# Kernel tuning notes

Measured on AMD Instinct MI355X. Metric: run time of the kernel, lower is better.

Reference implementation:

```python
import jax, jax.numpy as jnp
import numpy as np

B, S, D = 512, 200, 512
NQ, NC, NQD, NCD = 10000, 500, 101, 101


def _linear_params(key, fin, fout):
    # torch nn.Linear default init: U(-1/sqrt(fin), 1/sqrt(fin)); store W as (in,out)
    k1, k2 = jax.random.split(key)
    bound = 1.0 / np.sqrt(fin)
    W = jax.random.uniform(k1, (fin, fout), minval=-bound, maxval=bound, dtype=jnp.float32)
    b = jax.random.uniform(k2, (fout,), minval=-bound, maxval=bound, dtype=jnp.float32)
    return W, b


def setup_inputs() -> dict:
    key = jax.random.key(0)
    ks = jax.random.split(key, 16)
    inp = {
        'question_seq': jax.random.randint(ks[0], (B, S), 0, NQ),
        'concept_seq': jax.random.randint(ks[1], (B, S), 0, NC),
        'question_diff_seq': jax.random.randint(ks[2], (B, S), 0, NQD),
        'concept_diff_seq': jax.random.randint(ks[3], (B, S), 0, NCD),
        'correct_seq': jax.random.randint(ks[4], (B, S), 0, 2),
        'E_q': jax.random.normal(ks[5], (NQ, D), dtype=jnp.float32),
        'E_c': jax.random.normal(ks[6], (NC, D), dtype=jnp.float32),
        'E_qd': jax.random.normal(ks[7], (NQD, D), dtype=jnp.float32),
        'E_cd': jax.random.normal(ks[8], (NCD, D), dtype=jnp.float32),
        'E_corr': jax.random.normal(ks[9], (2, D), dtype=jnp.float32),
    }
    inp['W_x'], inp['b_x'] = _linear_params(ks[10], 4 * D, D)
    inp['W_s1'], inp['b_s1'] = _linear_params(ks[11], D, D)
    inp['W_s2'], inp['b_s2'] = _linear_params(ks[12], D, D)
    inp['W_p1'], inp['b_p1'] = _linear_params(ks[13], 2 * D, D)
    inp['W_p2'], inp['b_p2'] = _linear_params(ks[14], 2 * D, D)
    inp['W_ki'], inp['b_ki'] = _linear_params(ks[15], 4 * D, D)
    # h_pre: xavier_uniform on a (B, D) tensor -> U(-a, a), a = sqrt(6/(B+D))
    a = np.sqrt(6.0 / (B + D))
    inp['h0'] = jax.random.uniform(jax.random.key(1), (B, D), minval=-a, maxval=a, dtype=jnp.float32)
    return inp


def reference(question_seq, concept_seq, question_diff_seq, concept_diff_seq, correct_seq,
              E_q, E_c, E_qd, E_cd, E_corr,
              W_x, b_x, W_s1, b_s1, W_s2, b_s2, W_p1, b_p1, W_p2, b_p2, W_ki, b_ki, h0):
    # embedding lookups: [B, S, D]
    qe = E_q[question_seq]
    ce = E_c[concept_seq]
    qde = E_qd[question_diff_seq]
    cde = E_cd[concept_diff_seq]
    corr = E_corr[correct_seq]

    # generate_x_MLP applied to concat of 4 embeddings, vectorized over all t: [B, S, D]
    x_all = jnp.concatenate([qe, ce, qde, cde], axis=-1) @ W_x + b_x

    # time-major slices for scan over t = 0 .. S-2
    def tm(a):  # [B, S, D] -> [S, B, D]
        return jnp.swapaxes(a, 0, 1)

    xs = (tm(x_all)[:-1], tm(x_all)[1:], tm(corr)[:-1], tm(qde)[:-1], tm(cde)[:-1])

    def step(h_pre, t_in):
        x_t, x_next, ce_t, qd_t, cd_t = t_in
        d = x_t - h_pre
        # dropout in eval mode = identity
        sdf = jax.nn.sigmoid(d @ W_s1 + b_s1) * jnp.tanh(d @ W_s2 + b_s2)
        pka_in = jnp.concatenate([sdf, ce_t], axis=-1)
        pka = jax.nn.sigmoid(pka_in @ W_p1 + b_p1) * jnp.tanh(pka_in @ W_p2 + b_p2)
        ki_in = jnp.concatenate([h_pre, ce_t, qd_t, cd_t], axis=-1)
        gamma = jax.nn.sigmoid(ki_in @ W_ki + b_ki)
        h = gamma * h_pre + (1.0 - gamma) * pka
        y_t = jax.nn.sigmoid(jnp.sum(x_next * h, axis=-1))  # [B]
        return h, y_t

    _, y_seq = jax.lax.scan(step, h0, xs)  # y_seq: [S-1, B]
    y = jnp.concatenate([y_seq.T, jnp.zeros((question_seq.shape[0], 1), dtype=y_seq.dtype)], axis=1)
    return y  # [B, S], last column 0 as in the torch code
```

## Files before the change

kernel.cpp:

```cpp
#include <hip/hip_runtime.h>


typedef unsigned short u16;
using f32x4 = __attribute__((ext_vector_type(4))) float;
using bf16x8 = __attribute__((ext_vector_type(8))) short;

#define DEV static __device__ __forceinline__

#define Bv 512
#define Sv 200

DEV u16 f2bf(float f) {
  unsigned int u = __float_as_uint(f);
  unsigned int r = (u + 0x7fffu + ((u >> 16) & 1u)) >> 16;
  return (u16)r;
}
DEV float bf2f(u16 h) { return __uint_as_float(((unsigned int)h) << 16); }
DEV float sigm(float x) { return 1.0f / (1.0f + __expf(-x)); }
DEV float tanh_(float x) {
  x = fmaxf(fminf(x, 15.f), -15.f);
  float e = __expf(2.0f * x);
  return (e - 1.0f) / (e + 1.0f);
}
DEV f32x4 MF(bf16x8 a, bf16x8 b, f32x4 c) {
  return __builtin_amdgcn_mfma_f32_16x16x32_bf16(a, b, c, 0, 0, 0);
}

union LDU { f32x4 f; bf16x8 b; };
DEV void ld16v(f32x4* d, const u16* p) {
  asm volatile("global_load_dwordx4 %0, %1, off sc1" : "=v"(*d) : "v"(p));
}
DEV void st2v(u16* p, u16 v) {
  unsigned w = v;
  asm volatile("global_store_short %0, %1, off sc1" : : "v"(p), "v"(w) : "memory");
}
DEV void waitv0() {
  asm volatile("s_waitcnt vmcnt(0)" ::: "memory");
  __builtin_amdgcn_sched_barrier(0);
}

template <int NB, bool AF32>
DEV void gemm_tiles(const void* __restrict__ Aptr, int mvalid,
                    const u16* __restrict__ BT0, const u16* __restrict__ BT1,
                    u16* ldsA, u16* ldsB0, u16* ldsB1, int tid,
                    f32x4* acc0, f32x4* acc1) {
  const int lane = tid & 63, wid = tid >> 6;
  const int fr = lane & 15, fq = lane >> 4;
  const int srow = tid >> 2, sseg = tid & 3;

  for (int kt = 0; kt < 16; ++kt) {
    const int k0 = kt * 32;
    {
      bf16x8 pack;
      if constexpr (AF32) {
        if (srow < mvalid) {
          const float4* ap = (const float4*)((const float*)Aptr + (size_t)srow * 512 + k0 + sseg * 8);
          float4 v0 = ap[0], v1 = ap[1];
          pack[0] = (short)f2bf(v0.x); pack[1] = (short)f2bf(v0.y);
          pack[2] = (short)f2bf(v0.z); pack[3] = (short)f2bf(v0.w);
          pack[4] = (short)f2bf(v1.x); pack[5] = (short)f2bf(v1.y);
          pack[6] = (short)f2bf(v1.z); pack[7] = (short)f2bf(v1.w);
        } else {
          for (int j = 0; j < 8; ++j) pack[j] = 0;
        }
      } else {
        pack = *(const bf16x8*)((const u16*)Aptr + (size_t)srow * 512 + k0 + sseg * 8);
      }
      *(bf16x8*)&ldsA[srow * 40 + sseg * 8] = pack;
      *(bf16x8*)&ldsB0[srow * 40 + sseg * 8] =
          *(const bf16x8*)(BT0 + (size_t)srow * 512 + k0 + sseg * 8);
      if constexpr (NB == 2)
        *(bf16x8*)&ldsB1[srow * 40 + sseg * 8] =
            *(const bf16x8*)(BT1 + (size_t)srow * 512 + k0 + sseg * 8);
    }
    __syncthreads();
    bf16x8 a = *(const bf16x8*)&ldsA[(wid * 16 + fr) * 40 + fq * 8];
#pragma unroll
    for (int ni = 0; ni < 4; ++ni) {
      bf16x8 b0 = *(const bf16x8*)&ldsB0[(ni * 16 + fr) * 40 + fq * 8];
      acc0[ni] = MF(a, b0, acc0[ni]);
      if constexpr (NB == 2) {
        bf16x8 b1 = *(const bf16x8*)&ldsB1[(ni * 16 + fr) * 40 + fq * 8];
        acc1[ni] = MF(a, b1, acc1[ni]);
      }
    }
    __syncthreads();
  }
}

template <bool F32OUT>
__global__ __launch_bounds__(256) void gemm_table_k(const float* __restrict__ A, int M,
                                                    const u16* __restrict__ BT,
                                                    const float* __restrict__ bias,
                                                    void* __restrict__ C) {
  __shared__ u16 ldsA[64 * 40], ldsB[64 * 40];
  const int m0 = blockIdx.x * 64, n0 = blockIdx.y * 64;
  const int tid = threadIdx.x;
  f32x4 acc[4] = {};
  gemm_tiles<1, true>(A + (size_t)m0 * 512, M - m0, BT + (size_t)n0 * 512, nullptr,
                      ldsA, ldsB, nullptr, tid, acc, nullptr);
  const int lane = tid & 63, wid = tid >> 6, fr = lane & 15, fq = lane >> 4;
#pragma unroll
  for (int ni = 0; ni < 4; ++ni) {
    int col = n0 + ni * 16 + fr;
    float bv = bias ? bias[col] : 0.f;
#pragma unroll
    for (int r = 0; r < 4; ++r) {
      int row = m0 + wid * 16 + fq * 4 + r;
      if (row < M) {
        float v = acc[ni][r] + bv;
        if constexpr (F32OUT)
          ((float*)C)[(size_t)row * 512 + col] = v;
        else
          ((u16*)C)[(size_t)row * 512 + col] = f2bf(v);
      }
    }
  }
}

__global__ __launch_bounds__(256) void convT_k(const float* __restrict__ src, u16* __restrict__ dst) {
  __shared__ float tile[32][33];
  const int bi = blockIdx.x, bj = blockIdx.y;
  const int tx = threadIdx.x & 31, ty = threadIdx.x >> 5;
#pragma unroll
  for (int r = 0; r < 4; ++r)
    tile[ty + 8 * r][tx] = src[(size_t)(bj * 32 + ty + 8 * r) * 512 + bi * 32 + tx];
  __syncthreads();
#pragma unroll
  for (int r = 0; r < 4; ++r)
    dst[(size_t)(bi * 32 + ty + 8 * r) * 512 + bj * 32 + tx] = f2bf(tile[tx][ty + 8 * r]);
}

__global__ __launch_bounds__(256) void seqT_k(
    const int* __restrict__ q, const int* __restrict__ c, const int* __restrict__ qd,
    const int* __restrict__ cd, const int* __restrict__ corr,
    int* __restrict__ qT, int* __restrict__ cT, int* __restrict__ qdT,
    int* __restrict__ cdT, int* __restrict__ corrT) {
  const int i = blockIdx.x * 256 + threadIdx.x;
  const int b = i / Sv, t = i % Sv;
  const int o = t * Bv + b;
  qT[o] = q[i]; cT[o] = c[i]; qdT[o] = qd[i]; cdT[o] = cd[i]; corrT[o] = corr[i];
}

__global__ __launch_bounds__(256) void prologue_k(
    const float* __restrict__ h0, const int* __restrict__ qT, const int* __restrict__ cT,
    const int* __restrict__ qdT, const int* __restrict__ cdT,
    const float* __restrict__ XQ, const float* __restrict__ XC, const float* __restrict__ XQD,
    const float* __restrict__ XCD, u16* __restrict__ hb, u16* __restrict__ d_buf,
    unsigned* __restrict__ flags) {
  const int i = blockIdx.x * 256 + threadIdx.x;
  if (i < 4096) flags[i] = 0u;
  const int b = i >> 9, col = i & 511;
  float h = h0[i];
  int qi = qT[b], cci = cT[b], qdi = qdT[b], cdi = cdT[b];
  float x = XQ[(size_t)qi * 512 + col] + XC[(size_t)cci * 512 + col] +
            XQD[(size_t)qdi * 512 + col] + XCD[(size_t)cdi * 512 + col];
  hb[i] = f2bf(h);
  d_buf[i] = f2bf(x - h);
}

DEV void load_wslice32(const u16* __restrict__ src, u16* dst, int n0, int tid) {
  for (int i = tid; i < 2048; i += 256) {
    int q = i & 3, kc = (i >> 2) & 15, c = i >> 6;
    int slot = c * 4 + (q ^ (c & 3) ^ ((c >> 2) & 3));
    *(bf16x8*)&dst[kc * 1024 + slot * 8] =
        *(const bf16x8*)&src[(size_t)(n0 + c) * 512 + kc * 32 + q * 8];
  }
}

DEV void mg_arrive(unsigned* myslot, unsigned phase, int tid) {
  waitv0();
  __syncthreads();
  __builtin_amdgcn_fence(__ATOMIC_RELEASE, "workgroup");
  if (tid == 0)
    __hip_atomic_store(myslot, phase, __ATOMIC_RELAXED, __HIP_MEMORY_SCOPE_AGENT);
}
DEV void mg_wait(unsigned* mgslots, unsigned phase, int tid) {
  if (tid < 16) {
    while (__hip_atomic_load(&mgslots[tid * 16], __ATOMIC_RELAXED,
                             __HIP_MEMORY_SCOPE_AGENT) < phase)
      __builtin_amdgcn_s_sleep(0);
  }
  __syncthreads();
  __builtin_amdgcn_fence(__ATOMIC_ACQUIRE, "workgroup");
}

__global__ __launch_bounds__(256, 1) void scan_k(
    const u16* __restrict__ Ws1T, const u16* __restrict__ Ws2T, const u16* __restrict__ WkihT,
    const u16* __restrict__ Wp1aT, const u16* __restrict__ Wp2aT,
    const float* __restrict__ b_s1, const float* __restrict__ b_s2,
    const u16* __restrict__ Kcorr, const u16* __restrict__ Kqd, const u16* __restrict__ Kcd,
    const u16* __restrict__ P1c, const u16* __restrict__ P2c,
    const int* __restrict__ qT, const int* __restrict__ cT, const int* __restrict__ qdT,
    const int* __restrict__ cdT, const int* __restrict__ corrT,
    const float* __restrict__ XQ, const float* __restrict__ XC, const float* __restrict__ XQD,
    const float* __restrict__ XCD, const float* __restrict__ h0,
    u16* __restrict__ sdf, u16* __restrict__ dbuf, u16* __restrict__ hb,
    float* __restrict__ dotpart, unsigned* __restrict__ flags) {
  __shared__ u16 wlds[32768];
  const int bid = blockIdx.x;
  const int mg = (bid & 7) | ((bid >> 7) << 3);
  const int ns = (bid >> 3) & 15;
  const int n0 = ns * 32;
  const int tid = threadIdx.x, lane = tid & 63, w = tid >> 6;
  const int rt = w >> 1, ct = w & 1;
  const int fr = lane & 15, fq = lane >> 4;

  load_wslice32(Ws1T, wlds,          n0, tid);
  load_wslice32(Ws2T, wlds + 16384,  n0, tid);

  const int col = n0 + ct * 16 + fr;
  const float bs1 = b_s1[col], bs2 = b_s2[col];
  const float kco0 = bf2f(Kcorr[col]), kco1 = bf2f(Kcorr[512 + col]);
  const float p1c0 = bf2f(P1c[col]),   p1c1 = bf2f(P1c[512 + col]);
  const float p2c0 = bf2f(P2c[col]),   p2c1 = bf2f(P2c[512 + col]);

  const int crow0 = mg * 32 + rt * 16 + fq * 4;
  const size_t aoff = (size_t)(mg * 32 + rt * 16 + fr) * 512 + fq * 8;
  const int slotr = (ct * 16 + fr) * 4 + (fq ^ (fr & 3) ^ ((fr >> 2) & 3));
  const u16* wb = wlds + slotr * 8;

  bf16x8 wkf[16], wp1f[16], wp2f[16];
#pragma unroll
  for (int kc = 0; kc < 16; ++kc) {
    wkf[kc]  = *(const bf16x8*)(WkihT + (size_t)col * 512 + kc * 32 + fq * 8);
    wp1f[kc] = *(const bf16x8*)(Wp1aT + (size_t)col * 512 + kc * 32 + fq * 8);
    wp2f[kc] = *(const bf16x8*)(Wp2aT + (size_t)col * 512 + kc * 32 + fq * 8);
  }

  unsigned* myslot  = flags + (mg * 16 + ns) * 16;
  unsigned* mgslots = flags + mg * 16 * 16;

  float hl[4];
#pragma unroll
  for (int r = 0; r < 4; ++r) hl[r] = h0[(size_t)(crow0 + r) * 512 + col];
  int cis[4];
  float kbias[4];
#pragma unroll
  for (int r = 0; r < 4; ++r) {
    const int row = crow0 + r;
    int ci = corrT[row], qdi = qdT[row], cdi = cdT[row];
    cis[r] = ci;
    kbias[r] = (ci ? kco1 : kco0) + bf2f(Kqd[qdi * 512 + col]) + bf2f(Kcd[cdi * 512 + col]);
  }
  __syncthreads();

  for (int t = 0; t < Sv - 1; ++t) {
    LDU av[16], ah[16];
    __builtin_amdgcn_sched_barrier(0);
#pragma unroll
    for (int kc = 0; kc < 16; ++kc) ld16v(&av[kc].f, dbuf + aoff + kc * 32);
#pragma unroll
    for (int kc = 0; kc < 16; ++kc) ld16v(&ah[kc].f, hb + aoff + kc * 32);
    waitv0();
    f32x4 a1 = {}, a2 = {}, ag = {};
#pragma unroll
    for (int kc = 0; kc < 16; ++kc) {
      a1 = MF(av[kc].b, *(const bf16x8*)(wb + kc * 1024), a1);
      a2 = MF(av[kc].b, *(const bf16x8*)(wb + 16384 + kc * 1024), a2);
      ag = MF(ah[kc].b, wkf[kc], ag);
    }
    float g[4];
#pragma unroll
    for (int r = 0; r < 4; ++r) {
      g[r] = sigm(ag[r] + kbias[r]);
      st2v(&sdf[(size_t)(crow0 + r) * 512 + col], f2bf(sigm(a1[r] + bs1) * tanh_(a2[r] + bs2)));
    }
    mg_arrive(myslot, (unsigned)(2 * t + 1), tid);
    float xv[4];
#pragma unroll
    for (int r = 0; r < 4; ++r) {
      const int row = crow0 + r;
      int qi   = qT[(t + 1) * Bv + row];
      int cci  = cT[(t + 1) * Bv + row];
      int qdi2 = qdT[(t + 1) * Bv + row];
      int cdi2 = cdT[(t + 1) * Bv + row];
      xv[r] = XQ[(size_t)qi * 512 + col] + XC[(size_t)cci * 512 + col] +
              XQD[(size_t)qdi2 * 512 + col] + XCD[(size_t)cdi2 * 512 + col];
    }
    mg_wait(mgslots, (unsigned)(2 * t + 1), tid);

    LDU as[16];
    __builtin_amdgcn_sched_barrier(0);
#pragma unroll
    for (int kc = 0; kc < 16; ++kc) ld16v(&as[kc].f, sdf + aoff + kc * 32);
    waitv0();
    f32x4 ap1 = {}, ap2 = {};
#pragma unroll
    for (int kc = 0; kc < 16; ++kc) {
      ap1 = MF(as[kc].b, wp1f[kc], ap1);
      ap2 = MF(as[kc].b, wp2f[kc], ap2);
    }
    float dots[4];
#pragma unroll
    for (int r = 0; r < 4; ++r) {
      const int row = crow0 + r;
      float pka = sigm(ap1[r] + (cis[r] ? p1c1 : p1c0)) *
                  tanh_(ap2[r] + (cis[r] ? p2c1 : p2c0));
      float hn = g[r] * hl[r] + (1.f - g[r]) * pka;
      hl[r] = hn;
      st2v(&hb[(size_t)row * 512 + col],   f2bf(hn));
      st2v(&dbuf[(size_t)row * 512 + col], f2bf(xv[r] - hn));
      dots[r] = xv[r] * hn;
    }
    mg_arrive(myslot, (unsigned)(2 * t + 2), tid);
#pragma unroll
    for (int r = 0; r < 4; ++r) {
      float v = dots[r];
      v += __shfl_xor(v, 1);
      v += __shfl_xor(v, 2);
      v += __shfl_xor(v, 4);
      v += __shfl_xor(v, 8);
      if (fr == 0) dotpart[((size_t)t * Bv + crow0 + r) * 32 + ns * 2 + ct] = v;
    }
    if (t < Sv - 2) {
#pragma unroll
      for (int r = 0; r < 4; ++r) {
        const int row = crow0 + r;
        int ci = corrT[(t + 1) * Bv + row];
        int qdi = qdT[(t + 1) * Bv + row];
        int cdi = cdT[(t + 1) * Bv + row];
        cis[r] = ci;
        kbias[r] = (ci ? kco1 : kco0) + bf2f(Kqd[qdi * 512 + col]) +
                   bf2f(Kcd[cdi * 512 + col]);
      }
    }
    mg_wait(mgslots, (unsigned)(2 * t + 2), tid);
  }
}

__global__ __launch_bounds__(256) void finalize_k(const float* __restrict__ dotpart,
                                                  float* __restrict__ y) {
  const int i = blockIdx.x * 256 + threadIdx.x;
  const int b = i / Sv, t = i % Sv;
  float v = 0.f;
  if (t < Sv - 1) {
    const float4* p = (const float4*)&dotpart[((size_t)t * Bv + b) * 32];
    float s = 0.f;
#pragma unroll
    for (int k = 0; k < 8; ++k) {
      float4 q = p[k];
      s += q.x + q.y + q.z + q.w;
    }
    v = sigm(s);
  }
  y[i] = v;
}

extern "C" void kernel_launch(void* const* d_in, const int* in_sizes, int n_in,
                              void* d_out, int out_size, void* d_ws, size_t ws_size,
                              hipStream_t stream) {
  (void)in_sizes; (void)n_in; (void)out_size; (void)ws_size;
  const int* q_seq    = (const int*)d_in[0];
  const int* c_seq    = (const int*)d_in[1];
  const int* qd_seq   = (const int*)d_in[2];
  const int* cd_seq   = (const int*)d_in[3];
  const int* corr_seq = (const int*)d_in[4];
  const float* E_q    = (const float*)d_in[5];
  const float* E_c    = (const float*)d_in[6];
  const float* E_qd   = (const float*)d_in[7];
  const float* E_cd   = (const float*)d_in[8];
  const float* E_corr = (const float*)d_in[9];
  const float* W_x  = (const float*)d_in[10];
  const float* b_x  = (const float*)d_in[11];
  const float* W_s1 = (const float*)d_in[12];
  const float* b_s1 = (const float*)d_in[13];
  const float* W_s2 = (const float*)d_in[14];
  const float* b_s2 = (const float*)d_in[15];
  const float* W_p1 = (const float*)d_in[16];
  const float* b_p1 = (const float*)d_in[17];
  const float* W_p2 = (const float*)d_in[18];
  const float* b_p2 = (const float*)d_in[19];
  const float* W_ki = (const float*)d_in[20];
  const float* b_ki = (const float*)d_in[21];
  const float* h0   = (const float*)d_in[22];
  float* y = (float*)d_out;

  char* ws = (char*)d_ws;
  size_t off = 0;
  auto alloc = [&](size_t bytes) -> void* {
    void* p = ws + off;
    off += (bytes + 255) & ~(size_t)255;
    return p;
  };
  const size_t WSZ = 512 * 512 * sizeof(u16);
  u16* WxTq  = (u16*)alloc(WSZ);
  u16* WxTc  = (u16*)alloc(WSZ);
  u16* WxTqd = (u16*)alloc(WSZ);
  u16* WxTcd = (u16*)alloc(WSZ);
  u16* Ws1T  = (u16*)alloc(WSZ);
  u16* Ws2T  = (u16*)alloc(WSZ);
  u16* WkihT = (u16*)alloc(WSZ);
  u16* WkiTco = (u16*)alloc(WSZ);
  u16* WkiTqd = (u16*)alloc(WSZ);
  u16* WkiTcd = (u16*)alloc(WSZ);
  u16* Wp1aT = (u16*)alloc(WSZ);
  u16* Wp1hT = (u16*)alloc(WSZ);
  u16* Wp2aT = (u16*)alloc(WSZ);
  u16* Wp2hT = (u16*)alloc(WSZ);
  float* XQf  = (float*)alloc((size_t)10000 * 512 * 4);
  float* XCf  = (float*)alloc((size_t)500 * 512 * 4);
  float* XQDf = (float*)alloc((size_t)101 * 512 * 4);
  float* XCDf = (float*)alloc((size_t)101 * 512 * 4);
  u16* Kcorr = (u16*)alloc((size_t)2 * 512 * 2);
  u16* Kqd   = (u16*)alloc((size_t)101 * 512 * 2);
  u16* Kcd   = (u16*)alloc((size_t)101 * 512 * 2);
  u16* P1c   = (u16*)alloc((size_t)2 * 512 * 2);
  u16* P2c   = (u16*)alloc((size_t)2 * 512 * 2);
  u16* sdf   = (u16*)alloc((size_t)512 * 512 * 2);
  u16* d_buf = (u16*)alloc((size_t)512 * 512 * 2);
  u16* hb    = (u16*)alloc((size_t)512 * 512 * 2);
  float* dotpart = (float*)alloc((size_t)199 * 512 * 32 * 4);
  int* qT    = (int*)alloc((size_t)Sv * Bv * 4);
  int* cT    = (int*)alloc((size_t)Sv * Bv * 4);
  int* qdT   = (int*)alloc((size_t)Sv * Bv * 4);
  int* cdT   = (int*)alloc((size_t)Sv * Bv * 4);
  int* corrT = (int*)alloc((size_t)Sv * Bv * 4);
  unsigned* flags = (unsigned*)alloc(8192 * 4);

  dim3 blk(256);
  dim3 tg(16, 16);
  convT_k<<<tg, blk, 0, stream>>>(W_x + 0 * 512 * 512, WxTq);
  convT_k<<<tg, blk, 0, stream>>>(W_x + 1 * 512 * 512, WxTc);
  convT_k<<<tg, blk, 0, stream>>>(W_x + 2 * 512 * 512, WxTqd);
  convT_k<<<tg, blk, 0, stream>>>(W_x + 3 * 512 * 512, WxTcd);
  convT_k<<<tg, blk, 0, stream>>>(W_s1, Ws1T);
  convT_k<<<tg, blk, 0, stream>>>(W_s2, Ws2T);
  convT_k<<<tg, blk, 0, stream>>>(W_ki + 0 * 512 * 512, WkihT);
  convT_k<<<tg, blk, 0, stream>>>(W_ki + 1 * 512 * 512, WkiTco);
  convT_k<<<tg, blk, 0, stream>>>(W_ki + 2 * 512 * 512, WkiTqd);
  convT_k<<<tg, blk, 0, stream>>>(W_ki + 3 * 512 * 512, WkiTcd);
  convT_k<<<tg, blk, 0, stream>>>(W_p1 + 0 * 512 * 512, Wp1aT);
  convT_k<<<tg, blk, 0, stream>>>(W_p1 + 1 * 512 * 512, Wp1hT);
  convT_k<<<tg, blk, 0, stream>>>(W_p2 + 0 * 512 * 512, Wp2aT);
  convT_k<<<tg, blk, 0, stream>>>(W_p2 + 1 * 512 * 512, Wp2hT);

  gemm_table_k<true><<<dim3(157, 8), blk, 0, stream>>>(E_q, 10000, WxTq, nullptr, XQf);
  gemm_table_k<true><<<dim3(8, 8), blk, 0, stream>>>(E_c, 500, WxTc, b_x, XCf);
  gemm_table_k<true><<<dim3(2, 8), blk, 0, stream>>>(E_qd, 101, WxTqd, nullptr, XQDf);
  gemm_table_k<true><<<dim3(2, 8), blk, 0, stream>>>(E_cd, 101, WxTcd, nullptr, XCDf);
  gemm_table_k<false><<<dim3(1, 8), blk, 0, stream>>>(E_corr, 2, WkiTco, b_ki, Kcorr);
  gemm_table_k<false><<<dim3(2, 8), blk, 0, stream>>>(E_qd, 101, WkiTqd, nullptr, Kqd);
  gemm_table_k<false><<<dim3(2, 8), blk, 0, stream>>>(E_cd, 101, WkiTcd, nullptr, Kcd);
  gemm_table_k<false><<<dim3(1, 8), blk, 0, stream>>>(E_corr, 2, Wp1hT, b_p1, P1c);
  gemm_table_k<false><<<dim3(1, 8), blk, 0, stream>>>(E_corr, 2, Wp2hT, b_p2, P2c);

  seqT_k<<<dim3(400), blk, 0, stream>>>(q_seq, c_seq, qd_seq, cd_seq, corr_seq,
                                        qT, cT, qdT, cdT, corrT);
  prologue_k<<<dim3(1024), blk, 0, stream>>>(h0, qT, cT, qdT, cdT, XQf, XCf, XQDf, XCDf,
                                             hb, d_buf, flags);

  {
    const u16 *a0 = Ws1T, *a1 = Ws2T, *a2 = WkihT, *a3 = Wp1aT, *a4 = Wp2aT;
    const float *a5 = b_s1, *a6 = b_s2;
    const u16 *a7 = Kcorr, *a8 = Kqd, *a9 = Kcd, *a10 = P1c, *a11 = P2c;
    const int *a12 = qT, *a13 = cT, *a14 = qdT, *a15 = cdT, *a16 = corrT;
    const float *a17 = XQf, *a18 = XCf, *a19 = XQDf, *a20 = XCDf, *a21 = h0;
    u16 *a22 = sdf, *a23 = d_buf, *a24 = hb;
    float* a25 = dotpart;
    unsigned* a26 = flags;
    void* args[] = {&a0, &a1, &a2, &a3, &a4, &a5, &a6, &a7, &a8, &a9, &a10, &a11,
                    &a12, &a13, &a14, &a15, &a16, &a17, &a18, &a19, &a20, &a21,
                    &a22, &a23, &a24, &a25, &a26};
    hipError_t e = hipLaunchCooperativeKernel((void*)scan_k, dim3(256), dim3(256),
                                              args, 0, stream);
    if (e != hipSuccess) {
      scan_k<<<dim3(256), dim3(256), 0, stream>>>(Ws1T, Ws2T, WkihT, Wp1aT, Wp2aT,
                                                  b_s1, b_s2, Kcorr, Kqd, Kcd, P1c, P2c,
                                                  qT, cT, qdT, cdT, corrT,
                                                  XQf, XCf, XQDf, XCDf, h0,
                                                  sdf, d_buf, hb, dotpart, flags);
    }
  }

  finalize_k<<<dim3(400), blk, 0, stream>>>(dotpart, y);
}
```

Measured before the change: 2.452 ms.

## Split d@W_s into precomputed x-table projections minus h@W_s

Uses linearity so that (x - h)@W_s1 and (x - h)@W_s2 become x@W_s minus h@W_s. The x@W_s part is precomputed per embedding table (q, c, qd, cd, with the bias folded into the c table) and gathered per step. Inside the scan the same h fragments now feed all three MFMA chains, so the per-step d buffer no longer has to be loaded and stored. The cost is eight extra table GEMMs, including two over the 10000-row question table, plus eight extra bf16 gathers per row per step. Summing four bf16-rounded partial products also changes rounding behaviour.

```diff
diff --git a/kernel.cpp b/kernel.cpp
--- a/kernel.cpp
+++ b/kernel.cpp
@@ -143,20 +143,10 @@
 }
 
 __global__ __launch_bounds__(256) void prologue_k(
-    const float* __restrict__ h0, const int* __restrict__ qT, const int* __restrict__ cT,
-    const int* __restrict__ qdT, const int* __restrict__ cdT,
-    const float* __restrict__ XQ, const float* __restrict__ XC, const float* __restrict__ XQD,
-    const float* __restrict__ XCD, u16* __restrict__ hb, u16* __restrict__ d_buf,
-    unsigned* __restrict__ flags) {
+    const float* __restrict__ h0, u16* __restrict__ hb, unsigned* __restrict__ flags) {
   const int i = blockIdx.x * 256 + threadIdx.x;
   if (i < 4096) flags[i] = 0u;
-  const int b = i >> 9, col = i & 511;
-  float h = h0[i];
-  int qi = qT[b], cci = cT[b], qdi = qdT[b], cdi = cdT[b];
-  float x = XQ[(size_t)qi * 512 + col] + XC[(size_t)cci * 512 + col] +
-            XQD[(size_t)qdi * 512 + col] + XCD[(size_t)cdi * 512 + col];
-  hb[i] = f2bf(h);
-  d_buf[i] = f2bf(x - h);
+  hb[i] = f2bf(h0[i]);
 }
 
 DEV void load_wslice32(const u16* __restrict__ src, u16* dst, int n0, int tid) {
@@ -188,14 +178,17 @@
 __global__ __launch_bounds__(256, 1) void scan_k(
     const u16* __restrict__ Ws1T, const u16* __restrict__ Ws2T, const u16* __restrict__ WkihT,
     const u16* __restrict__ Wp1aT, const u16* __restrict__ Wp2aT,
-    const float* __restrict__ b_s1, const float* __restrict__ b_s2,
     const u16* __restrict__ Kcorr, const u16* __restrict__ Kqd, const u16* __restrict__ Kcd,
     const u16* __restrict__ P1c, const u16* __restrict__ P2c,
+    const u16* __restrict__ XQS1, const u16* __restrict__ XQS2,
+    const u16* __restrict__ XCS1, const u16* __restrict__ XCS2,
+    const u16* __restrict__ XQDS1, const u16* __restrict__ XQDS2,
+    const u16* __restrict__ XCDS1, const u16* __restrict__ XCDS2,
     const int* __restrict__ qT, const int* __restrict__ cT, const int* __restrict__ qdT,
     const int* __restrict__ cdT, const int* __restrict__ corrT,
     const float* __restrict__ XQ, const float* __restrict__ XC, const float* __restrict__ XQD,
     const float* __restrict__ XCD, const float* __restrict__ h0,
-    u16* __restrict__ sdf, u16* __restrict__ dbuf, u16* __restrict__ hb,
+    u16* __restrict__ sdf, u16* __restrict__ hb,
     float* __restrict__ dotpart, unsigned* __restrict__ flags) {
   __shared__ u16 wlds[32768];
   const int bid = blockIdx.x;
@@ -210,7 +203,6 @@
   load_wslice32(Ws2T, wlds + 16384,  n0, tid);
 
   const int col = n0 + ct * 16 + fr;
-  const float bs1 = b_s1[col], bs2 = b_s2[col];
   const float kco0 = bf2f(Kcorr[col]), kco1 = bf2f(Kcorr[512 + col]);
   const float p1c0 = bf2f(P1c[col]),   p1c1 = bf2f(P1c[512 + col]);
   const float p2c0 = bf2f(P2c[col]),   p2c1 = bf2f(P2c[512 + col]);
@@ -234,37 +226,43 @@
   float hl[4];
 #pragma unroll
   for (int r = 0; r < 4; ++r) hl[r] = h0[(size_t)(crow0 + r) * 512 + col];
+
+  float xs1[4], xs2[4], kbias[4];
   int cis[4];
-  float kbias[4];
 #pragma unroll
   for (int r = 0; r < 4; ++r) {
     const int row = crow0 + r;
-    int ci = corrT[row], qdi = qdT[row], cdi = cdT[row];
+    int qi = qT[row], cci = cT[row], qdi = qdT[row], cdi = cdT[row];
+    int ci = corrT[row];
+    xs1[r] = bf2f(XQS1[(size_t)qi * 512 + col]) + bf2f(XCS1[(size_t)cci * 512 + col]) +
+             bf2f(XQDS1[(size_t)qdi * 512 + col]) + bf2f(XCDS1[(size_t)cdi * 512 + col]);
+    xs2[r] = bf2f(XQS2[(size_t)qi * 512 + col]) + bf2f(XCS2[(size_t)cci * 512 + col]) +
+             bf2f(XQDS2[(size_t)qdi * 512 + col]) + bf2f(XCDS2[(size_t)cdi * 512 + col]);
     cis[r] = ci;
     kbias[r] = (ci ? kco1 : kco0) + bf2f(Kqd[qdi * 512 + col]) + bf2f(Kcd[cdi * 512 + col]);
   }
   __syncthreads();
 
   for (int t = 0; t < Sv - 1; ++t) {
-    LDU av[16], ah[16];
+    LDU ah[16];
     __builtin_amdgcn_sched_barrier(0);
-#pragma unroll
-    for (int kc = 0; kc < 16; ++kc) ld16v(&av[kc].f, dbuf + aoff + kc * 32);
 #pragma unroll
     for (int kc = 0; kc < 16; ++kc) ld16v(&ah[kc].f, hb + aoff + kc * 32);
     waitv0();
     f32x4 a1 = {}, a2 = {}, ag = {};
 #pragma unroll
     for (int kc = 0; kc < 16; ++kc) {
-      a1 = MF(av[kc].b, *(const bf16x8*)(wb + kc * 1024), a1);
-      a2 = MF(av[kc].b, *(const bf16x8*)(wb + 16384 + kc * 1024), a2);
+      a1 = MF(ah[kc].b, *(const bf16x8*)(wb + kc * 1024), a1);
+      a2 = MF(ah[kc].b, *(const bf16x8*)(wb + 16384 + kc * 1024), a2);
       ag = MF(ah[kc].b, wkf[kc], ag);
     }
     float g[4];
 #pragma unroll
     for (int r = 0; r < 4; ++r) {
       g[r] = sigm(ag[r] + kbias[r]);
-      st2v(&sdf[(size_t)(crow0 + r) * 512 + col], f2bf(sigm(a1[r] + bs1) * tanh_(a2[r] + bs2)));
+      float u1 = xs1[r] - a1[r];
+      float u2 = xs2[r] - a2[r];
+      st2v(&sdf[(size_t)(crow0 + r) * 512 + col], f2bf(sigm(u1) * tanh_(u2)));
     }
     mg_arrive(myslot, (unsigned)(2 * t + 1), tid);
     float xv[4];
@@ -277,6 +275,10 @@
       int cdi2 = cdT[(t + 1) * Bv + row];
       xv[r] = XQ[(size_t)qi * 512 + col] + XC[(size_t)cci * 512 + col] +
               XQD[(size_t)qdi2 * 512 + col] + XCD[(size_t)cdi2 * 512 + col];
+      xs1[r] = bf2f(XQS1[(size_t)qi * 512 + col]) + bf2f(XCS1[(size_t)cci * 512 + col]) +
+               bf2f(XQDS1[(size_t)qdi2 * 512 + col]) + bf2f(XCDS1[(size_t)cdi2 * 512 + col]);
+      xs2[r] = bf2f(XQS2[(size_t)qi * 512 + col]) + bf2f(XCS2[(size_t)cci * 512 + col]) +
+               bf2f(XQDS2[(size_t)qdi2 * 512 + col]) + bf2f(XCDS2[(size_t)cdi2 * 512 + col]);
     }
     mg_wait(mgslots, (unsigned)(2 * t + 1), tid);
 
@@ -299,8 +301,7 @@
                   tanh_(ap2[r] + (cis[r] ? p2c1 : p2c0));
       float hn = g[r] * hl[r] + (1.f - g[r]) * pka;
       hl[r] = hn;
-      st2v(&hb[(size_t)row * 512 + col],   f2bf(hn));
-      st2v(&dbuf[(size_t)row * 512 + col], f2bf(xv[r] - hn));
+      st2v(&hb[(size_t)row * 512 + col], f2bf(hn));
       dots[r] = xv[r] * hn;
     }
     mg_arrive(myslot, (unsigned)(2 * t + 2), tid);
@@ -402,13 +403,20 @@
   float* XCf  = (float*)alloc((size_t)500 * 512 * 4);
   float* XQDf = (float*)alloc((size_t)101 * 512 * 4);
   float* XCDf = (float*)alloc((size_t)101 * 512 * 4);
+  u16* XQS1  = (u16*)alloc((size_t)10000 * 512 * 2);
+  u16* XQS2  = (u16*)alloc((size_t)10000 * 512 * 2);
+  u16* XCS1  = (u16*)alloc((size_t)500 * 512 * 2);
+  u16* XCS2  = (u16*)alloc((size_t)500 * 512 * 2);
+  u16* XQDS1 = (u16*)alloc((size_t)101 * 512 * 2);
+  u16* XQDS2 = (u16*)alloc((size_t)101 * 512 * 2);
+  u16* XCDS1 = (u16*)alloc((size_t)101 * 512 * 2);
+  u16* XCDS2 = (u16*)alloc((size_t)101 * 512 * 2);
   u16* Kcorr = (u16*)alloc((size_t)2 * 512 * 2);
   u16* Kqd   = (u16*)alloc((size_t)101 * 512 * 2);
   u16* Kcd   = (u16*)alloc((size_t)101 * 512 * 2);
   u16* P1c   = (u16*)alloc((size_t)2 * 512 * 2);
   u16* P2c   = (u16*)alloc((size_t)2 * 512 * 2);
   u16* sdf   = (u16*)alloc((size_t)512 * 512 * 2);
-  u16* d_buf = (u16*)alloc((size_t)512 * 512 * 2);
   u16* hb    = (u16*)alloc((size_t)512 * 512 * 2);
   float* dotpart = (float*)alloc((size_t)199 * 512 * 32 * 4);
   int* qT    = (int*)alloc((size_t)Sv * Bv * 4);
@@ -439,6 +447,16 @@
   gemm_table_k<true><<<dim3(8, 8), blk, 0, stream>>>(E_c, 500, WxTc, b_x, XCf);
   gemm_table_k<true><<<dim3(2, 8), blk, 0, stream>>>(E_qd, 101, WxTqd, nullptr, XQDf);
   gemm_table_k<true><<<dim3(2, 8), blk, 0, stream>>>(E_cd, 101, WxTcd, nullptr, XCDf);
+
+  gemm_table_k<false><<<dim3(157, 8), blk, 0, stream>>>(XQf, 10000, Ws1T, nullptr, XQS1);
+  gemm_table_k<false><<<dim3(157, 8), blk, 0, stream>>>(XQf, 10000, Ws2T, nullptr, XQS2);
+  gemm_table_k<false><<<dim3(8, 8), blk, 0, stream>>>(XCf, 500, Ws1T, b_s1, XCS1);
+  gemm_table_k<false><<<dim3(8, 8), blk, 0, stream>>>(XCf, 500, Ws2T, b_s2, XCS2);
+  gemm_table_k<false><<<dim3(2, 8), blk, 0, stream>>>(XQDf, 101, Ws1T, nullptr, XQDS1);
+  gemm_table_k<false><<<dim3(2, 8), blk, 0, stream>>>(XQDf, 101, Ws2T, nullptr, XQDS2);
+  gemm_table_k<false><<<dim3(2, 8), blk, 0, stream>>>(XCDf, 101, Ws1T, nullptr, XCDS1);
+  gemm_table_k<false><<<dim3(2, 8), blk, 0, stream>>>(XCDf, 101, Ws2T, nullptr, XCDS2);
+
   gemm_table_k<false><<<dim3(1, 8), blk, 0, stream>>>(E_corr, 2, WkiTco, b_ki, Kcorr);
   gemm_table_k<false><<<dim3(2, 8), blk, 0, stream>>>(E_qd, 101, WkiTqd, nullptr, Kqd);
   gemm_table_k<false><<<dim3(2, 8), blk, 0, stream>>>(E_cd, 101, WkiTcd, nullptr, Kcd);
@@ -447,29 +465,32 @@
 
   seqT_k<<<dim3(400), blk, 0, stream>>>(q_seq, c_seq, qd_seq, cd_seq, corr_seq,
                                         qT, cT, qdT, cdT, corrT);
-  prologue_k<<<dim3(1024), blk, 0, stream>>>(h0, qT, cT, qdT, cdT, XQf, XCf, XQDf, XCDf,
-                                             hb, d_buf, flags);
+  prologue_k<<<dim3(1024), blk, 0, stream>>>(h0, hb, flags);
 
   {
     const u16 *a0 = Ws1T, *a1 = Ws2T, *a2 = WkihT, *a3 = Wp1aT, *a4 = Wp2aT;
-    const float *a5 = b_s1, *a6 = b_s2;
-    const u16 *a7 = Kcorr, *a8 = Kqd, *a9 = Kcd, *a10 = P1c, *a11 = P2c;
-    const int *a12 = qT, *a13 = cT, *a14 = qdT, *a15 = cdT, *a16 = corrT;
-    const float *a17 = XQf, *a18 = XCf, *a19 = XQDf, *a20 = XCDf, *a21 = h0;
-    u16 *a22 = sdf, *a23 = d_buf, *a24 = hb;
-    float* a25 = dotpart;
-    unsigned* a26 = flags;
-    void* args[] = {&a0, &a1, &a2, &a3, &a4, &a5, &a6, &a7, &a8, &a9, &a10, &a11,
-                    &a12, &a13, &a14, &a15, &a16, &a17, &a18, &a19, &a20, &a21,
-                    &a22, &a23, &a24, &a25, &a26};
+    const u16 *a5 = Kcorr, *a6 = Kqd, *a7 = Kcd, *a8 = P1c, *a9 = P2c;
+    const u16 *a10 = XQS1, *a11 = XQS2, *a12 = XCS1, *a13 = XCS2;
+    const u16 *a14 = XQDS1, *a15 = XQDS2, *a16 = XCDS1, *a17 = XCDS2;
+    const int *a18 = qT, *a19 = cT, *a20 = qdT, *a21 = cdT, *a22 = corrT;
+    const float *a23 = XQf, *a24 = XCf, *a25 = XQDf, *a26 = XCDf, *a27 = h0;
+    u16 *a28 = sdf, *a29 = hb;
+    float* a30 = dotpart;
+    unsigned* a31 = flags;
+    void* args[] = {&a0, &a1, &a2, &a3, &a4, &a5, &a6, &a7, &a8, &a9,
+                    &a10, &a11, &a12, &a13, &a14, &a15, &a16, &a17,
+                    &a18, &a19, &a20, &a21, &a22, &a23, &a24, &a25, &a26, &a27,
+                    &a28, &a29, &a30, &a31};
     hipError_t e = hipLaunchCooperativeKernel((void*)scan_k, dim3(256), dim3(256),
                                               args, 0, stream);
     if (e != hipSuccess) {
       scan_k<<<dim3(256), dim3(256), 0, stream>>>(Ws1T, Ws2T, WkihT, Wp1aT, Wp2aT,
-                                                  b_s1, b_s2, Kcorr, Kqd, Kcd, P1c, P2c,
+                                                  Kcorr, Kqd, Kcd, P1c, P2c,
+                                                  XQS1, XQS2, XCS1, XCS2,
+                                                  XQDS1, XQDS2, XCDS1, XCDS2,
                                                   qT, cT, qdT, cdT, corrT,
                                                   XQf, XCf, XQDf, XCDf, h0,
-                                                  sdf, d_buf, hb, dotpart, flags);
+                                                  sdf, hb, dotpart, flags);
     }
   }
 
```

Measured after the change: 2.324 ms. -5.2%, faster.
